# Optimization experiments

Hardware: AMD Instinct MI355X
Metric: run time of the kernel (lower is better)

The kernel has to match this reference:

```python
import jax, jax.numpy as jnp
import numpy as np

B, S, H, E, L = 8, 512, 768, 8, 2
SPAN, ATTR = 5, 31
EPS = 1e-5


def _layernorm(x, g, b):
    mu = jnp.mean(x, axis=-1, keepdims=True)
    var = jnp.mean(jnp.square(x - mu), axis=-1, keepdims=True)
    return g * (x - mu) * jax.lax.rsqrt(var + EPS) + b


def setup_inputs() -> dict:
    key = jax.random.key(0)
    ks = iter(jax.random.split(key, 32))

    def unif(k, shape, bound):
        return jax.random.uniform(k, shape, jnp.float32, -bound, bound)

    b3d = float(np.sqrt(6.0 / (H * E + H * E)))   # xavier for [H,H,E]
    bH = float(1.0 / np.sqrt(H))
    inp = {
        "share_hidden": jax.random.normal(next(ks), (B, S, H), jnp.float32),
        "span_hidden": jax.random.normal(next(ks), (B, S, H), jnp.float32),
        "attr_hidden": jax.random.normal(next(ks), (B, S, H), jnp.float32),
        # per-layer params stacked on leading axis L; expert axis order: (shared, task1, task2)
        "ln_g": jnp.ones((L, 3, H), jnp.float32),
        "ln_b": jnp.zeros((L, 3, H), jnp.float32),
        "W_exp": unif(next(ks), (L, 3, H, H, E), b3d),
        "b_exp": unif(next(ks), (L, 3, H, E), bH),
        "Wg_sh": unif(next(ks), (L, H, 3 * E), bH),
        "bg_sh": unif(next(ks), (L, 3 * E), bH),
        "Wg_t1": unif(next(ks), (L, H, 2 * E), bH),
        "bg_t1": unif(next(ks), (L, 2 * E), bH),
        "Wg_t2": unif(next(ks), (L, H, 2 * E), bH),
        "bg_t2": unif(next(ks), (L, 2 * E), bH),
        "W_span": unif(next(ks), (H, SPAN), bH),
        "b_span": unif(next(ks), (SPAN,), bH),
        "W_as": unif(next(ks), (H, ATTR), bH),
        "b_as": unif(next(ks), (ATTR,), bH),
        "W_ae": unif(next(ks), (H, ATTR), bH),
        "b_ae": unif(next(ks), (ATTR,), bH),
    }
    return inp


def reference(share_hidden, span_hidden, attr_hidden, ln_g, ln_b, W_exp, b_exp,
              Wg_sh, bg_sh, Wg_t1, bg_t1, Wg_t2, bg_t2,
              W_span, b_span, W_as, b_as, W_ae, b_ae):
    act = lambda x: jax.nn.gelu(x, approximate=False)  # torch F.gelu default is exact
    h_sh, h_t1, h_t2 = share_hidden, span_hidden, attr_hidden
    for l in range(L):
        x_sh = _layernorm(h_sh, ln_g[l, 0], ln_b[l, 0])
        x_t1 = _layernorm(h_t1, ln_g[l, 1], ln_b[l, 1])
        x_t2 = _layernorm(h_t2, ln_g[l, 2], ln_b[l, 2])
        # batched expert projections: [B,S,H] x [H,H,E] -> [B,S,H,E]
        e_sh = act(jnp.einsum('bsh,hxe->bsxe', x_sh, W_exp[l, 0]) + b_exp[l, 0])
        e_t1 = act(jnp.einsum('bsh,hxe->bsxe', x_t1, W_exp[l, 1]) + b_exp[l, 1])
        e_t2 = act(jnp.einsum('bsh,hxe->bsxe', x_t2, W_exp[l, 2]) + b_exp[l, 2])
        # gates
        g_sh = jax.nn.softmax(x_sh @ Wg_sh[l] + bg_sh[l], axis=-1)   # [B,S,3E]
        g_t1 = jax.nn.softmax(x_t1 @ Wg_t1[l] + bg_t1[l], axis=-1)   # [B,S,2E]
        g_t2 = jax.nn.softmax(x_t2 @ Wg_t2[l] + bg_t2[l], axis=-1)   # [B,S,2E]
        # weighted combine over concatenated expert axes (concat order matches torch code)
        o_sh = jnp.einsum('bse,bsxe->bsx', g_sh, jnp.concatenate([e_t1, e_sh, e_t2], axis=-1))
        o_t1 = jnp.einsum('bse,bsxe->bsx', g_t1, jnp.concatenate([e_t1, e_sh], axis=-1))
        o_t2 = jnp.einsum('bse,bsxe->bsx', g_t2, jnp.concatenate([e_t2, e_sh], axis=-1))
        # residual accumulation (progressive_layered_extraction)
        h_sh = h_sh + o_sh
        h_t1 = h_t1 + o_t1
        h_t2 = h_t2 + o_t2
    span_logits = h_t1 @ W_span + b_span
    attr_start_logits = h_t2 @ W_as + b_as
    attr_end_logits = h_t2 @ W_ae + b_ae
    return (span_logits, attr_start_logits, attr_end_logits)
```

## Files before the change

kernel.cpp:

```cpp
#include <hip/hip_runtime.h>
#include <hip/hip_bf16.h>
#include <math.h>

#define M_ 4096
#define N_ 6144
#define K_ 768
#define KP 832
#define H_ 768
#define L_ 2
#define NT 13

using bf16x8 = __attribute__((ext_vector_type(8))) short;
using f32x4  = __attribute__((ext_vector_type(4))) float;

__device__ __forceinline__ unsigned short f2bf(float f) {
  unsigned int u = __builtin_bit_cast(unsigned int, f);
  u += 0x7FFFu + ((u >> 16) & 1u);
  return (unsigned short)(u >> 16);
}

__device__ __forceinline__ float bf2f(unsigned short u) {
  return __builtin_bit_cast(float, (unsigned int)u << 16);
}

__device__ __forceinline__ float gelu_fast(float x) {
  float u2 = x * (1.5957691f + 0.07135481f * x * x);
  return x / (1.f + __expf(-u2));
}

__device__ __forceinline__ void gload_lds16(const void* g, void* l) {
  __builtin_amdgcn_global_load_lds(
      (__attribute__((address_space(1))) unsigned int*)(uintptr_t)g,
      (__attribute__((address_space(3))) unsigned int*)(unsigned int)(uintptr_t)l,
      16, 0, 0);
}

__global__ __launch_bounds__(256) void conv_w(const float* __restrict__ W,
                                              const float* __restrict__ bias,
                                              short* __restrict__ Wb) {
  __shared__ float tile[64][65];
  const int z = blockIdx.z;
  const int n0 = blockIdx.x * 64;
  const int k0 = blockIdx.y * 64;
  const size_t inb  = (size_t)z * K_ * N_;
  const size_t outb = (size_t)z * N_ * KP;
  const int tid = threadIdx.x;
  const int c = tid & 63;
  const int r = tid >> 6;
#pragma unroll
  for (int p = 0; p < 16; ++p) {
    const int kk = p * 4 + r;
    tile[c][kk] = W[inb + (size_t)(k0 + kk) * N_ + n0 + c];
  }
  __syncthreads();
#pragma unroll
  for (int p = 0; p < 16; ++p) {
    const int nn = p * 4 + r;
    Wb[outb + (size_t)(n0 + nn) * KP + k0 + c] = (short)f2bf(tile[nn][c]);
  }
  if (blockIdx.y == 0) {
    const int row = tid >> 2, c0 = (tid & 3) * 16;
    short* dst = Wb + outb + (size_t)(n0 + row) * KP + 768 + c0;
    ushort4 vz; vz.x = 0; vz.y = 0; vz.z = 0; vz.w = 0;
    ushort4 v0 = vz;
    if (c0 == 0) v0.x = f2bf(bias[(size_t)z * N_ + n0 + row]);
    *(ushort4*)dst = v0;
    *(ushort4*)(dst + 4) = vz;
    *(ushort4*)(dst + 8) = vz;
    *(ushort4*)(dst + 12) = vz;
  }
}

__global__ __launch_bounds__(256, 4) void ln_gates(
    const float* __restrict__ in0, const float* __restrict__ in1,
    const float* __restrict__ in2,
    float* __restrict__ h,
    const unsigned short* __restrict__ part,
    int mode,
    short* __restrict__ xs,
    const float* __restrict__ ln_g,
    const float* __restrict__ ln_b,
    const float* __restrict__ Wg_sh, const float* __restrict__ bg_sh,
    const float* __restrict__ Wg_t1, const float* __restrict__ bg_t1,
    const float* __restrict__ Wg_t2, const float* __restrict__ bg_t2,
    float* __restrict__ gates)
{
  const int gw   = blockIdx.x * 4 + (threadIdx.x >> 6);
  const int t    = gw >> 12;
  const int row  = gw & 4095;
  const int lane = threadIdx.x & 63;
  const float* srow = (t == 0 ? in0 : (t == 1 ? in1 : in2)) + (size_t)row * H_;
  float* hrow = h + ((size_t)t * M_ + row) * H_;

  const size_t MH = (size_t)M_ * H_;
  const unsigned short *pa = nullptr, *pb = nullptr, *pc = nullptr;
  if (mode) {
    if (t == 0)      { pa = part + (size_t)row * H_;          pb = part + 3 * MH + (size_t)row * H_; pc = part + 5 * MH + (size_t)row * H_; }
    else if (t == 1) { pa = part + 1 * MH + (size_t)row * H_; pb = part + 4 * MH + (size_t)row * H_; }
    else             { pa = part + 2 * MH + (size_t)row * H_; pb = part + 6 * MH + (size_t)row * H_; }
  }

  float x[12];
  float sum = 0.f, ss = 0.f;
#pragma unroll
  for (int q = 0; q < 3; ++q) {
    const int o = q * 256 + lane * 4;
    float4 v = *(const float4*)(srow + o);
    if (mode) {
      ushort4 a4 = *(const ushort4*)(pa + o);
      ushort4 b4 = *(const ushort4*)(pb + o);
      v.x += bf2f(a4.x) + bf2f(b4.x);
      v.y += bf2f(a4.y) + bf2f(b4.y);
      v.z += bf2f(a4.z) + bf2f(b4.z);
      v.w += bf2f(a4.w) + bf2f(b4.w);
      if (t == 0) {
        ushort4 c4 = *(const ushort4*)(pc + o);
        v.x += bf2f(c4.x); v.y += bf2f(c4.y); v.z += bf2f(c4.z); v.w += bf2f(c4.w);
      }
      *(float4*)(hrow + o) = v;
    }
    x[q * 4 + 0] = v.x; x[q * 4 + 1] = v.y; x[q * 4 + 2] = v.z; x[q * 4 + 3] = v.w;
    sum += v.x + v.y + v.z + v.w;
    ss  += v.x * v.x + v.y * v.y + v.z * v.z + v.w * v.w;
  }
#pragma unroll
  for (int m = 1; m < 64; m <<= 1) { sum += __shfl_xor(sum, m); ss += __shfl_xor(ss, m); }
  const float mean = sum * (1.f / 768.f);
  float var = ss * (1.f / 768.f) - mean * mean;
  var = var < 0.f ? 0.f : var;
  const float rstd = rsqrtf(var + 1e-5f);

  const float* ga = ln_g + (size_t)t * H_;
  const float* be = ln_b + (size_t)t * H_;
  short* xrow = xs + ((size_t)t * M_ + row) * KP;
#pragma unroll
  for (int q = 0; q < 3; ++q) {
    float4 g4 = *(const float4*)(ga + q * 256 + lane * 4);
    float4 b4 = *(const float4*)(be + q * 256 + lane * 4);
    float y0 = g4.x * (x[q * 4 + 0] - mean) * rstd + b4.x;
    float y1 = g4.y * (x[q * 4 + 1] - mean) * rstd + b4.y;
    float y2 = g4.z * (x[q * 4 + 2] - mean) * rstd + b4.z;
    float y3 = g4.w * (x[q * 4 + 3] - mean) * rstd + b4.w;
    x[q * 4 + 0] = y0; x[q * 4 + 1] = y1; x[q * 4 + 2] = y2; x[q * 4 + 3] = y3;
    ushort4 st; st.x = f2bf(y0); st.y = f2bf(y1); st.z = f2bf(y2); st.w = f2bf(y3);
    *(ushort4*)(xrow + q * 256 + lane * 4) = st;
  }
  if (lane < 16) {
    ushort4 z; z.x = (lane == 0) ? 0x3F80 : 0; z.y = 0; z.z = 0; z.w = 0;
    *(ushort4*)(xrow + 768 + lane * 4) = z;
  }

  const float* Wg; const float* bg;
  if (t == 0)      { Wg = Wg_sh; bg = bg_sh; }
  else if (t == 1) { Wg = Wg_t1; bg = bg_t1; }
  else             { Wg = Wg_t2; bg = bg_t2; }
  const int NG = (t == 0) ? 24 : 16;

  float p[24];
#pragma unroll
  for (int j = 0; j < 24; ++j) p[j] = 0.f;
#pragma unroll
  for (int q = 0; q < 3; ++q)
#pragma unroll
    for (int jj = 0; jj < 4; ++jj) {
      const int i = q * 256 + lane * 4 + jj;
      const float xv = x[q * 4 + jj];
      const float* wrow = Wg + (size_t)i * NG;
#pragma unroll
      for (int j = 0; j < 16; ++j) p[j] += xv * wrow[j];
      if (t == 0) {
#pragma unroll
        for (int j = 16; j < 24; ++j) p[j] += xv * wrow[j];
      }
    }
#pragma unroll
  for (int j = 0; j < 16; ++j)
#pragma unroll
    for (int m = 1; m < 64; m <<= 1) p[j] += __shfl_xor(p[j], m);
  if (t == 0) {
#pragma unroll
    for (int j = 16; j < 24; ++j)
#pragma unroll
      for (int m = 1; m < 64; m <<= 1) p[j] += __shfl_xor(p[j], m);
  }
  float mx = -1e30f;
#pragma unroll
  for (int j = 0; j < 16; ++j) { p[j] += bg[j]; mx = fmaxf(mx, p[j]); }
  if (t == 0) {
#pragma unroll
    for (int j = 16; j < 24; ++j) { p[j] += bg[j]; mx = fmaxf(mx, p[j]); }
  }
  float s = 0.f;
#pragma unroll
  for (int j = 0; j < 16; ++j) { p[j] = __expf(p[j] - mx); s += p[j]; }
  if (t == 0) {
#pragma unroll
    for (int j = 16; j < 24; ++j) { p[j] = __expf(p[j] - mx); s += p[j]; }
  }
  const float inv = 1.f / s;

  float* grow;
  if (t == 0)      grow = gates + (size_t)row * 24;
  else if (t == 1) grow = gates + (size_t)M_ * 24 + (size_t)row * 16;
  else             grow = gates + (size_t)M_ * 24 + (size_t)M_ * 16 + (size_t)row * 16;
  if (lane == 0) {
#pragma unroll
    for (int j = 0; j < 16; ++j) grow[j] = p[j] * inv;
    if (t == 0) {
#pragma unroll
      for (int j = 16; j < 24; ++j) grow[j] = p[j] * inv;
    }
  }
}

__global__ __launch_bounds__(256, 3) void expert_gemm(
    const short* __restrict__ xs,
    const short* __restrict__ Wb,
    const float* __restrict__ g_sh,
    const float* __restrict__ g_t1,
    const float* __restrict__ g_t2,
    unsigned short* __restrict__ part)
{
  __shared__ short lds[16384];

  const int bid = blockIdx.x;
  const int xcd = bid & 7;
  const int idx = bid >> 3;
  const int t   = idx / 192;
  const int r2  = idx - t * 192;
  const int mt  = r2 / 6;
  const int m0  = mt * 128;
  const int n0  = (xcd * 6 + (r2 - mt * 6)) * 128;

  const short* A  = xs + (size_t)t * M_ * KP;
  const short* Bt = Wb + (size_t)t * N_ * KP;

  const int tid = threadIdx.x;
  const int w = tid >> 6, l = tid & 63;
  const int wr = w >> 1, wc = w & 1;

  const int lr = l & 15, cg = l >> 4;
  const int fx = lr >> 1;
  const int slot0 = ((cg ^ fx) << 3);
  const int slot1 = (((4 + cg) ^ fx) << 3);
  const int aoff = wr * 4096 + lr * 64;
  const int boff = 8192 + wc * 4096 + lr * 64;

  f32x4 acc[4][4];
#pragma unroll
  for (int i = 0; i < 4; ++i)
#pragma unroll
    for (int j = 0; j < 4; ++j) acc[i][j] = (f32x4){0.f, 0.f, 0.f, 0.f};

  for (int kt = 0; kt < NT; ++kt) {
    __syncthreads();
#pragma unroll
    for (int q = 0; q < 4; ++q) {
      const int row = w * 32 + q * 8 + (l >> 3);
      const int fq = (q * 4 + (l >> 4)) & 7;
      const int csw = ((l & 7) ^ fq) << 3;
      gload_lds16(A  + (size_t)(m0 + row) * KP + kt * 64 + csw, &lds[(w * 32 + q * 8) * 64]);
      gload_lds16(Bt + (size_t)(n0 + row) * KP + kt * 64 + csw, &lds[8192 + (w * 32 + q * 8) * 64]);
    }
    __syncthreads();

    bf16x8 a[4][2], b[4][2];
#pragma unroll
    for (int fm = 0; fm < 4; ++fm) {
      a[fm][0] = *(const bf16x8*)&lds[aoff + fm * 1024 + slot0];
      a[fm][1] = *(const bf16x8*)&lds[aoff + fm * 1024 + slot1];
    }
#pragma unroll
    for (int fn = 0; fn < 4; ++fn) {
      b[fn][0] = *(const bf16x8*)&lds[boff + fn * 1024 + slot0];
      b[fn][1] = *(const bf16x8*)&lds[boff + fn * 1024 + slot1];
    }
    __builtin_amdgcn_s_setprio(1);
#pragma unroll
    for (int ks = 0; ks < 2; ++ks)
#pragma unroll
      for (int fm = 0; fm < 4; ++fm)
#pragma unroll
        for (int fn = 0; fn < 4; ++fn)
          acc[fm][fn] = __builtin_amdgcn_mfma_f32_16x16x32_bf16(a[fm][ks], b[fn][ks], acc[fm][fn], 0, 0, 0);
    __builtin_amdgcn_s_setprio(0);
  }
  __syncthreads();

  const size_t MH = (size_t)M_ * H_;
  const float *gpA, *gpB, *gpC = nullptr;
  unsigned short *ppA, *ppB, *ppC = nullptr;
  int ldA, ldB, ldC = 16, offA, offB, offC = 0, ntg;
  if (t == 0) {
    gpA = g_sh; ldA = 24; offA = 8; ppA = part;
    gpB = g_t1; ldB = 16; offB = 8; ppB = part + 1 * MH;
    gpC = g_t2; ldC = 16; offC = 8; ppC = part + 2 * MH; ntg = 3;
  } else if (t == 1) {
    gpA = g_sh; ldA = 24; offA = 0; ppA = part + 3 * MH;
    gpB = g_t1; ldB = 16; offB = 0; ppB = part + 4 * MH; ntg = 2;
  } else {
    gpA = g_sh; ldA = 24; offA = 16; ppA = part + 5 * MH;
    gpB = g_t2; ldB = 16; offB = 0;  ppB = part + 6 * MH; ntg = 2;
  }
  float* wtile = (float*)lds + w * 1040;
  const int xbase = (n0 + wc * 64) >> 3;
  const int xloc = l & 7;

#pragma unroll
  for (int fm = 0; fm < 4; ++fm) {
    asm volatile("s_waitcnt lgkmcnt(0)" ::: "memory");
#pragma unroll
    for (int fn = 0; fn < 4; ++fn)
#pragma unroll
      for (int r = 0; r < 4; ++r)
        wtile[(cg * 4 + r) * 65 + fn * 16 + lr] = gelu_fast(acc[fm][fn][r]);
    asm volatile("s_waitcnt lgkmcnt(0)" ::: "memory");

    float v[2][8];
    int gm[2];
#pragma unroll
    for (int p = 0; p < 2; ++p) {
      const int mloc = p * 8 + (l >> 3);
      float4 v0 = *(const float4*)&wtile[mloc * 65 + xloc * 8];
      float4 v1 = *(const float4*)&wtile[mloc * 65 + xloc * 8 + 4];
      v[p][0] = v0.x; v[p][1] = v0.y; v[p][2] = v0.z; v[p][3] = v0.w;
      v[p][4] = v1.x; v[p][5] = v1.y; v[p][6] = v1.z; v[p][7] = v1.w;
      gm[p] = m0 + wr * 64 + fm * 16 + mloc;
    }

#define DO_STREAM(gp, ldg, offg, pp)                                          \
    {                                                                         \
      _Pragma("unroll")                                                       \
      for (int p = 0; p < 2; ++p) {                                           \
        const float* gr = (gp) + (size_t)gm[p] * (ldg) + (offg);              \
        float4 ga = *(const float4*)gr;                                       \
        float4 gb = *(const float4*)(gr + 4);                                 \
        float o = ga.x * v[p][0] + ga.y * v[p][1] + ga.z * v[p][2]            \
                + ga.w * v[p][3] + gb.x * v[p][4] + gb.y * v[p][5]            \
                + gb.z * v[p][6] + gb.w * v[p][7];                            \
        (pp)[(size_t)gm[p] * H_ + xbase + xloc] = f2bf(o);                    \
      }                                                                       \
    }
    DO_STREAM(gpA, ldA, offA, ppA);
    DO_STREAM(gpB, ldB, offB, ppB);
    if (ntg == 3) DO_STREAM(gpC, ldC, offC, ppC);
#undef DO_STREAM
  }
}

__global__ __launch_bounds__(128) void heads(
    const float* __restrict__ h,
    const unsigned short* __restrict__ part,
    const float* __restrict__ Wspan, const float* __restrict__ bspan,
    const float* __restrict__ Was,   const float* __restrict__ bas,
    const float* __restrict__ Wae,   const float* __restrict__ bae,
    float* __restrict__ out)
{
  const int row = blockIdx.x;
  __shared__ float s1[768], s2[768];
  const size_t MH = (size_t)M_ * H_;
  const float* h1 = h + ((size_t)M_ + row) * H_;
  const float* h2 = h + ((size_t)2 * M_ + row) * H_;
  const unsigned short* p1a = part + 1 * MH + (size_t)row * H_;
  const unsigned short* p1b = part + 4 * MH + (size_t)row * H_;
  const unsigned short* p2a = part + 2 * MH + (size_t)row * H_;
  const unsigned short* p2b = part + 6 * MH + (size_t)row * H_;
  for (int i = threadIdx.x; i < 768; i += 128) {
    s1[i] = h1[i] + bf2f(p1a[i]) + bf2f(p1b[i]);
    s2[i] = h2[i] + bf2f(p2a[i]) + bf2f(p2b[i]);
  }
  __syncthreads();
  const int j = threadIdx.x;
  const float* W; const float* src; float bias; float* op; int ldw;
  if (j < 5)       { W = Wspan + j;      src = s1; bias = bspan[j];  op = out + (size_t)row * 5 + j;                ldw = 5;  }
  else if (j < 36) { W = Was + (j - 5);  src = s2; bias = bas[j-5];  op = out + 20480 + (size_t)row * 31 + (j-5);   ldw = 31; }
  else if (j < 67) { W = Wae + (j - 36); src = s2; bias = bae[j-36]; op = out + 147456 + (size_t)row * 31 + (j-36); ldw = 31; }
  else return;
  float acc = bias;
  for (int i = 0; i < 768; ++i) acc += src[i] * W[(size_t)i * ldw];
  *op = acc;
}

extern "C" void kernel_launch(void* const* d_in, const int* in_sizes, int n_in,
                              void* d_out, int out_size, void* d_ws, size_t ws_size,
                              hipStream_t stream) {
  (void)in_sizes; (void)n_in; (void)out_size; (void)ws_size;
  const float* share  = (const float*)d_in[0];
  const float* span   = (const float*)d_in[1];
  const float* attr   = (const float*)d_in[2];
  const float* ln_g   = (const float*)d_in[3];
  const float* ln_b   = (const float*)d_in[4];
  const float* W_exp  = (const float*)d_in[5];
  const float* b_exp  = (const float*)d_in[6];
  const float* Wg_sh  = (const float*)d_in[7];
  const float* bg_sh  = (const float*)d_in[8];
  const float* Wg_t1  = (const float*)d_in[9];
  const float* bg_t1  = (const float*)d_in[10];
  const float* Wg_t2  = (const float*)d_in[11];
  const float* bg_t2  = (const float*)d_in[12];
  const float* W_span = (const float*)d_in[13];
  const float* b_span = (const float*)d_in[14];
  const float* W_as   = (const float*)d_in[15];
  const float* b_as   = (const float*)d_in[16];
  const float* W_ae   = (const float*)d_in[17];
  const float* b_ae   = (const float*)d_in[18];

  char* ws = (char*)d_ws;
  short* Wb = (short*)ws;
  size_t o = (size_t)3 * N_ * KP * 2;
  short* xs = (short*)(ws + o); o += (size_t)3 * M_ * KP * 2;
  float* h  = (float*)(ws + o); o += (size_t)3 * M_ * H_ * 4;
  float* gates = (float*)(ws + o); o += (size_t)M_ * (24 + 16 + 16) * 4;
  unsigned short* part = (unsigned short*)(ws + o);

  for (int l = 0; l < L_; ++l) {
    conv_w<<<dim3(96, 12, 3), 256, 0, stream>>>(
        W_exp + (size_t)l * 3 * K_ * N_, b_exp + (size_t)l * 3 * N_, Wb);
    ln_gates<<<3072, 256, 0, stream>>>(
        share, span, attr, h, part, l, xs,
        ln_g + (size_t)l * 3 * H_, ln_b + (size_t)l * 3 * H_,
        Wg_sh + (size_t)l * H_ * 24, bg_sh + (size_t)l * 24,
        Wg_t1 + (size_t)l * H_ * 16, bg_t1 + (size_t)l * 16,
        Wg_t2 + (size_t)l * H_ * 16, bg_t2 + (size_t)l * 16,
        gates);
    expert_gemm<<<4608, 256, 0, stream>>>(
        xs, Wb,
        gates, gates + (size_t)M_ * 24, gates + (size_t)M_ * 24 + (size_t)M_ * 16,
        part);
  }

  heads<<<4096, 128, 0, stream>>>(h, part, W_span, b_span, W_as, b_as, W_ae, b_ae,
                                  (float*)d_out);
}
```

Before: 591.8 us.

## Widen expert GEMM tile to 128x256 with triple-buffered async LDS pipeline

Doubles the expert GEMM block tile along N (128x256) and halves the K step to 32. The K loop becomes a three-stage ring buffer: global-to-LDS loads for step kt+2 are issued while step kt is computed, and vmcnt waits with a single barrier replace the two syncthreads per iteration. The goal is to hide global load latency and raise MFMA work per byte loaded. In exchange, LDS grows to about 72 KB and registers to 32 accumulators per wave, so occupancy drops to 2 blocks per CU and the grid is halved. The epilogue is remapped to the wider tile.

```diff
diff --git a/kernel.cpp b/kernel.cpp
--- a/kernel.cpp
+++ b/kernel.cpp
@@ -8,7 +8,7 @@
 #define KP 832
 #define H_ 768
 #define L_ 2
-#define NT 13
+#define NT 26
 
 using bf16x8 = __attribute__((ext_vector_type(8))) short;
 using f32x4  = __attribute__((ext_vector_type(4))) float;
@@ -213,7 +213,7 @@
   }
 }
 
-__global__ __launch_bounds__(256, 3) void expert_gemm(
+__global__ __launch_bounds__(256, 2) void expert_gemm(
     const short* __restrict__ xs,
     const short* __restrict__ Wb,
     const float* __restrict__ g_sh,
@@ -221,69 +221,83 @@
     const float* __restrict__ g_t2,
     unsigned short* __restrict__ part)
 {
-  __shared__ short lds[16384];
+  __shared__ short lds[36864];
 
   const int bid = blockIdx.x;
   const int xcd = bid & 7;
   const int idx = bid >> 3;
-  const int t   = idx / 192;
-  const int r2  = idx - t * 192;
-  const int mt  = r2 / 6;
+  const int t   = idx / 96;
+  const int r2  = idx - t * 96;
+  const int mt  = r2 / 3;
   const int m0  = mt * 128;
-  const int n0  = (xcd * 6 + (r2 - mt * 6)) * 128;
+  const int n0  = (xcd * 3 + (r2 - mt * 3)) * 256;
 
   const short* A  = xs + (size_t)t * M_ * KP;
   const short* Bt = Wb + (size_t)t * N_ * KP;
 
   const int tid = threadIdx.x;
   const int w = tid >> 6, l = tid & 63;
-  const int wr = w >> 1, wc = w & 1;
+  const int wr = w & 1, wc = w >> 1;
+
+  const int csw = (((l & 3) ^ ((l >> 3) & 3)) << 3);
+  const int lrow = l >> 2;
+  const short* As0 = A  + (size_t)(m0 +       w * 16 + lrow) * KP + csw;
+  const short* As1 = A  + (size_t)(m0 +  64 + w * 16 + lrow) * KP + csw;
+  const short* Bs0 = Bt + (size_t)(n0 +       w * 16 + lrow) * KP + csw;
+  const short* Bs1 = Bt + (size_t)(n0 +  64 + w * 16 + lrow) * KP + csw;
+  const short* Bs2 = Bt + (size_t)(n0 + 128 + w * 16 + lrow) * KP + csw;
+  const short* Bs3 = Bt + (size_t)(n0 + 192 + w * 16 + lrow) * KP + csw;
+  const int dstw = w * 512;
+
+  auto stage = [&](int kt) {
+    const int bb = (kt % 3) * 12288;
+    const int ko = kt * 32;
+    gload_lds16(As0 + ko, &lds[bb + dstw]);
+    gload_lds16(As1 + ko, &lds[bb + 2048 + dstw]);
+    gload_lds16(Bs0 + ko, &lds[bb + 4096 + dstw]);
+    gload_lds16(Bs1 + ko, &lds[bb + 6144 + dstw]);
+    gload_lds16(Bs2 + ko, &lds[bb + 8192 + dstw]);
+    gload_lds16(Bs3 + ko, &lds[bb + 10240 + dstw]);
+  };
 
   const int lr = l & 15, cg = l >> 4;
-  const int fx = lr >> 1;
-  const int slot0 = ((cg ^ fx) << 3);
-  const int slot1 = (((4 + cg) ^ fx) << 3);
-  const int aoff = wr * 4096 + lr * 64;
-  const int boff = 8192 + wc * 4096 + lr * 64;
-
-  f32x4 acc[4][4];
+  const int slot = ((cg ^ ((lr >> 1) & 3)) << 3);
+  const int aoff = (wr * 64 + lr) * 32 + slot;
+  const int boff = 4096 + (wc * 128 + lr) * 32 + slot;
+
+  f32x4 acc[4][8];
 #pragma unroll
   for (int i = 0; i < 4; ++i)
 #pragma unroll
-    for (int j = 0; j < 4; ++j) acc[i][j] = (f32x4){0.f, 0.f, 0.f, 0.f};
+    for (int j = 0; j < 8; ++j) acc[i][j] = (f32x4){0.f, 0.f, 0.f, 0.f};
+
+  stage(0); stage(1);
+  asm volatile("s_waitcnt vmcnt(6)" ::: "memory");
+  __builtin_amdgcn_s_barrier();
 
   for (int kt = 0; kt < NT; ++kt) {
-    __syncthreads();
-#pragma unroll
-    for (int q = 0; q < 4; ++q) {
-      const int row = w * 32 + q * 8 + (l >> 3);
-      const int fq = (q * 4 + (l >> 4)) & 7;
-      const int csw = ((l & 7) ^ fq) << 3;
-      gload_lds16(A  + (size_t)(m0 + row) * KP + kt * 64 + csw, &lds[(w * 32 + q * 8) * 64]);
-      gload_lds16(Bt + (size_t)(n0 + row) * KP + kt * 64 + csw, &lds[8192 + (w * 32 + q * 8) * 64]);
+    if (kt + 2 < NT) stage(kt + 2);
+    __builtin_amdgcn_sched_barrier(0);
+
+    const int bb = (kt % 3) * 12288;
+    bf16x8 a[4], b[8];
+#pragma unroll
+    for (int fm = 0; fm < 4; ++fm) a[fm] = *(const bf16x8*)&lds[bb + aoff + fm * 512];
+#pragma unroll
+    for (int fn = 0; fn < 8; ++fn) b[fn] = *(const bf16x8*)&lds[bb + boff + fn * 512];
+    __builtin_amdgcn_s_setprio(1);
+#pragma unroll
+    for (int fm = 0; fm < 4; ++fm)
+#pragma unroll
+      for (int fn = 0; fn < 8; ++fn)
+        acc[fm][fn] = __builtin_amdgcn_mfma_f32_16x16x32_bf16(a[fm], b[fn], acc[fm][fn], 0, 0, 0);
+    __builtin_amdgcn_s_setprio(0);
+
+    if (kt < NT - 1) {
+      if (kt + 2 < NT) asm volatile("s_waitcnt vmcnt(6)" ::: "memory");
+      else             asm volatile("s_waitcnt vmcnt(0)" ::: "memory");
+      __builtin_amdgcn_s_barrier();
     }
-    __syncthreads();
-
-    bf16x8 a[4][2], b[4][2];
-#pragma unroll
-    for (int fm = 0; fm < 4; ++fm) {
-      a[fm][0] = *(const bf16x8*)&lds[aoff + fm * 1024 + slot0];
-      a[fm][1] = *(const bf16x8*)&lds[aoff + fm * 1024 + slot1];
-    }
-#pragma unroll
-    for (int fn = 0; fn < 4; ++fn) {
-      b[fn][0] = *(const bf16x8*)&lds[boff + fn * 1024 + slot0];
-      b[fn][1] = *(const bf16x8*)&lds[boff + fn * 1024 + slot1];
-    }
-    __builtin_amdgcn_s_setprio(1);
-#pragma unroll
-    for (int ks = 0; ks < 2; ++ks)
-#pragma unroll
-      for (int fm = 0; fm < 4; ++fm)
-#pragma unroll
-        for (int fn = 0; fn < 4; ++fn)
-          acc[fm][fn] = __builtin_amdgcn_mfma_f32_16x16x32_bf16(a[fm][ks], b[fn][ks], acc[fm][fn], 0, 0, 0);
-    __builtin_amdgcn_s_setprio(0);
   }
   __syncthreads();
 
@@ -302,49 +316,41 @@
     gpA = g_sh; ldA = 24; offA = 16; ppA = part + 5 * MH;
     gpB = g_t2; ldB = 16; offB = 0;  ppB = part + 6 * MH; ntg = 2;
   }
-  float* wtile = (float*)lds + w * 1040;
-  const int xbase = (n0 + wc * 64) >> 3;
-  const int xloc = l & 7;
+  float* wtile = (float*)lds + w * 2112;
+  const int xloc = l >> 2;
+  const int mfr  = l & 3;
+  const int xcol = ((n0 + wc * 128) >> 3) + xloc;
 
 #pragma unroll
   for (int fm = 0; fm < 4; ++fm) {
     asm volatile("s_waitcnt lgkmcnt(0)" ::: "memory");
 #pragma unroll
-    for (int fn = 0; fn < 4; ++fn)
+    for (int fn = 0; fn < 8; ++fn)
 #pragma unroll
       for (int r = 0; r < 4; ++r)
-        wtile[(cg * 4 + r) * 65 + fn * 16 + lr] = gelu_fast(acc[fm][fn][r]);
+        wtile[(cg * 4 + r) * 132 + fn * 16 + lr] = gelu_fast(acc[fm][fn][r]);
     asm volatile("s_waitcnt lgkmcnt(0)" ::: "memory");
 
-    float v[2][8];
-    int gm[2];
-#pragma unroll
-    for (int p = 0; p < 2; ++p) {
-      const int mloc = p * 8 + (l >> 3);
-      float4 v0 = *(const float4*)&wtile[mloc * 65 + xloc * 8];
-      float4 v1 = *(const float4*)&wtile[mloc * 65 + xloc * 8 + 4];
-      v[p][0] = v0.x; v[p][1] = v0.y; v[p][2] = v0.z; v[p][3] = v0.w;
-      v[p][4] = v1.x; v[p][5] = v1.y; v[p][6] = v1.z; v[p][7] = v1.w;
-      gm[p] = m0 + wr * 64 + fm * 16 + mloc;
-    }
-
+#pragma unroll
+    for (int p = 0; p < 4; ++p) {
+      const int mloc = p * 4 + mfr;
+      const int gm = m0 + wr * 64 + fm * 16 + mloc;
+      float4 v0 = *(const float4*)&wtile[mloc * 132 + xloc * 8];
+      float4 v1 = *(const float4*)&wtile[mloc * 132 + xloc * 8 + 4];
 #define DO_STREAM(gp, ldg, offg, pp)                                          \
-    {                                                                         \
-      _Pragma("unroll")                                                       \
-      for (int p = 0; p < 2; ++p) {                                           \
-        const float* gr = (gp) + (size_t)gm[p] * (ldg) + (offg);              \
+      {                                                                       \
+        const float* gr = (gp) + (size_t)gm * (ldg) + (offg);                 \
         float4 ga = *(const float4*)gr;                                       \
         float4 gb = *(const float4*)(gr + 4);                                 \
-        float o = ga.x * v[p][0] + ga.y * v[p][1] + ga.z * v[p][2]            \
-                + ga.w * v[p][3] + gb.x * v[p][4] + gb.y * v[p][5]            \
-                + gb.z * v[p][6] + gb.w * v[p][7];                            \
-        (pp)[(size_t)gm[p] * H_ + xbase + xloc] = f2bf(o);                    \
-      }                                                                       \
+        float o = ga.x * v0.x + ga.y * v0.y + ga.z * v0.z + ga.w * v0.w       \
+                + gb.x * v1.x + gb.y * v1.y + gb.z * v1.z + gb.w * v1.w;      \
+        (pp)[(size_t)gm * H_ + xcol] = f2bf(o);                               \
+      }
+      DO_STREAM(gpA, ldA, offA, ppA);
+      DO_STREAM(gpB, ldB, offB, ppB);
+      if (ntg == 3) DO_STREAM(gpC, ldC, offC, ppC);
+#undef DO_STREAM
     }
-    DO_STREAM(gpA, ldA, offA, ppA);
-    DO_STREAM(gpB, ldB, offB, ppB);
-    if (ntg == 3) DO_STREAM(gpC, ldC, offC, ppC);
-#undef DO_STREAM
   }
 }
 
@@ -423,7 +429,7 @@
         Wg_t1 + (size_t)l * H_ * 16, bg_t1 + (size_t)l * 16,
         Wg_t2 + (size_t)l * H_ * 16, bg_t2 + (size_t)l * 16,
         gates);
-    expert_gemm<<<4608, 256, 0, stream>>>(
+    expert_gemm<<<2304, 256, 0, stream>>>(
         xs, Wb,
         gates, gates + (size_t)M_ * 24, gates + (size_t)M_ * 24 + (size_t)M_ * 16,
         part);
```

Measured after the change: 620.5 us. +4.8%, slower.

## Triple-buffer expert GEMM LDS tiles with async prefetch two stages ahead

Applied to the files above, without the earlier changes.

Replaces the load-then-sync loop of the expert GEMM with a 3-stage ring buffer in LDS. Each stage now covers a K-slice of 32 instead of 64, and global-to-LDS loads are issued two iterations ahead. Explicit vmcnt waits plus a single barrier per iteration replace the two __syncthreads. This is meant to hide global memory latency behind the MFMAs. In exchange it doubles the iteration count, uses 48KB of LDS instead of 32KB (which may limit occupancy at 3 blocks per CU), and changes the swizzle pattern.

```diff
diff --git a/kernel.cpp b/kernel.cpp
--- a/kernel.cpp
+++ b/kernel.cpp
@@ -8,7 +8,7 @@
 #define KP 832
 #define H_ 768
 #define L_ 2
-#define NT 13
+#define NT 26
 
 using bf16x8 = __attribute__((ext_vector_type(8))) short;
 using f32x4  = __attribute__((ext_vector_type(4))) float;
@@ -221,7 +221,7 @@
     const float* __restrict__ g_t2,
     unsigned short* __restrict__ part)
 {
-  __shared__ short lds[16384];
+  __shared__ short lds[24576];
 
   const int bid = blockIdx.x;
   const int xcd = bid & 7;
@@ -239,12 +239,27 @@
   const int w = tid >> 6, l = tid & 63;
   const int wr = w >> 1, wc = w & 1;
 
+  const int csw = (((l & 3) ^ ((l >> 3) & 3)) << 3);
+  const int lrow = l >> 2;
+  const short* As0 = A  + (size_t)(m0 +      w * 16 + lrow) * KP + csw;
+  const short* As1 = A  + (size_t)(m0 + 64 + w * 16 + lrow) * KP + csw;
+  const short* Bs0 = Bt + (size_t)(n0 +      w * 16 + lrow) * KP + csw;
+  const short* Bs1 = Bt + (size_t)(n0 + 64 + w * 16 + lrow) * KP + csw;
+  const int dstw = w * 512;
+
+  auto stage = [&](int kt) {
+    const int bb = (kt % 3) * 8192;
+    const int ko = kt * 32;
+    gload_lds16(As0 + ko, &lds[bb + dstw]);
+    gload_lds16(As1 + ko, &lds[bb + 2048 + dstw]);
+    gload_lds16(Bs0 + ko, &lds[bb + 4096 + dstw]);
+    gload_lds16(Bs1 + ko, &lds[bb + 6144 + dstw]);
+  };
+
   const int lr = l & 15, cg = l >> 4;
-  const int fx = lr >> 1;
-  const int slot0 = ((cg ^ fx) << 3);
-  const int slot1 = (((4 + cg) ^ fx) << 3);
-  const int aoff = wr * 4096 + lr * 64;
-  const int boff = 8192 + wc * 4096 + lr * 64;
+  const int slot = ((cg ^ ((lr >> 1) & 3)) << 3);
+  const int aoff = (wr * 64 + lr) * 32 + slot;
+  const int boff = 4096 + (wc * 64 + lr) * 32 + slot;
 
   f32x4 acc[4][4];
 #pragma unroll
@@ -252,38 +267,33 @@
 #pragma unroll
     for (int j = 0; j < 4; ++j) acc[i][j] = (f32x4){0.f, 0.f, 0.f, 0.f};
 
+  stage(0); stage(1);
+  asm volatile("s_waitcnt vmcnt(4)" ::: "memory");
+  __builtin_amdgcn_s_barrier();
+
   for (int kt = 0; kt < NT; ++kt) {
-    __syncthreads();
-#pragma unroll
-    for (int q = 0; q < 4; ++q) {
-      const int row = w * 32 + q * 8 + (l >> 3);
-      const int fq = (q * 4 + (l >> 4)) & 7;
-      const int csw = ((l & 7) ^ fq) << 3;
-      gload_lds16(A  + (size_t)(m0 + row) * KP + kt * 64 + csw, &lds[(w * 32 + q * 8) * 64]);
-      gload_lds16(Bt + (size_t)(n0 + row) * KP + kt * 64 + csw, &lds[8192 + (w * 32 + q * 8) * 64]);
-    }
-    __syncthreads();
-
-    bf16x8 a[4][2], b[4][2];
-#pragma unroll
-    for (int fm = 0; fm < 4; ++fm) {
-      a[fm][0] = *(const bf16x8*)&lds[aoff + fm * 1024 + slot0];
-      a[fm][1] = *(const bf16x8*)&lds[aoff + fm * 1024 + slot1];
-    }
-#pragma unroll
-    for (int fn = 0; fn < 4; ++fn) {
-      b[fn][0] = *(const bf16x8*)&lds[boff + fn * 1024 + slot0];
-      b[fn][1] = *(const bf16x8*)&lds[boff + fn * 1024 + slot1];
-    }
+    if (kt + 2 < NT) stage(kt + 2);
+    __builtin_amdgcn_sched_barrier(0);
+
+    const int bb = (kt % 3) * 8192;
+    bf16x8 a[4], b[4];
+#pragma unroll
+    for (int fm = 0; fm < 4; ++fm) a[fm] = *(const bf16x8*)&lds[bb + aoff + fm * 512];
+#pragma unroll
+    for (int fn = 0; fn < 4; ++fn) b[fn] = *(const bf16x8*)&lds[bb + boff + fn * 512];
     __builtin_amdgcn_s_setprio(1);
 #pragma unroll
-    for (int ks = 0; ks < 2; ++ks)
-#pragma unroll
-      for (int fm = 0; fm < 4; ++fm)
-#pragma unroll
-        for (int fn = 0; fn < 4; ++fn)
-          acc[fm][fn] = __builtin_amdgcn_mfma_f32_16x16x32_bf16(a[fm][ks], b[fn][ks], acc[fm][fn], 0, 0, 0);
+    for (int fm = 0; fm < 4; ++fm)
+#pragma unroll
+      for (int fn = 0; fn < 4; ++fn)
+        acc[fm][fn] = __builtin_amdgcn_mfma_f32_16x16x32_bf16(a[fm], b[fn], acc[fm][fn], 0, 0, 0);
     __builtin_amdgcn_s_setprio(0);
+
+    if (kt < NT - 1) {
+      if (kt + 2 < NT) asm volatile("s_waitcnt vmcnt(4) lgkmcnt(0)" ::: "memory");
+      else             asm volatile("s_waitcnt vmcnt(0) lgkmcnt(0)" ::: "memory");
+      __builtin_amdgcn_s_barrier();
+    }
   }
   __syncthreads();
 
```

Measured after the change: 623.3 us. +5.3%, slower.

## Stage gate weights in LDS as transposed bf16 and process two rows per wave

Applied to the files above, without the earlier changes.

The ln_gates kernel now loads each task's gate weight matrix once per block into shared memory, transposed and converted to bf16, so that each lane reads contiguous weights for its 12 input elements. Previously every lane read strided fp32 gate rows from global memory for each row. Each block now covers 8 rows (two per wave) and the grid is halved, which spreads the staging cost over more rows. In exchange it adds a block-level staging pass, 36KB of LDS per block, and bf16 rounding of the gate weights, which may slightly change the softmax outputs.

```diff
diff --git a/kernel.cpp b/kernel.cpp
--- a/kernel.cpp
+++ b/kernel.cpp
@@ -68,6 +68,38 @@
     *(ushort4*)(dst + 4) = vz;
     *(ushort4*)(dst + 8) = vz;
     *(ushort4*)(dst + 12) = vz;
+  }
+}
+
+template<int NG>
+__device__ __forceinline__ void gate_sm(const float x[12],
+    const unsigned short* Wlds, const float* __restrict__ bg,
+    float* __restrict__ grow, int lane) {
+  float p[NG];
+#pragma unroll
+  for (int j = 0; j < NG; ++j) {
+    const unsigned short* wr = Wlds + j * 768 + lane * 4;
+    ushort4 wa = *(const ushort4*)wr;
+    ushort4 wb = *(const ushort4*)(wr + 256);
+    ushort4 wc = *(const ushort4*)(wr + 512);
+    p[j] = bf2f(wa.x) * x[0] + bf2f(wa.y) * x[1] + bf2f(wa.z) * x[2]  + bf2f(wa.w) * x[3]
+         + bf2f(wb.x) * x[4] + bf2f(wb.y) * x[5] + bf2f(wb.z) * x[6]  + bf2f(wb.w) * x[7]
+         + bf2f(wc.x) * x[8] + bf2f(wc.y) * x[9] + bf2f(wc.z) * x[10] + bf2f(wc.w) * x[11];
+  }
+#pragma unroll
+  for (int j = 0; j < NG; ++j)
+#pragma unroll
+    for (int m = 1; m < 64; m <<= 1) p[j] += __shfl_xor(p[j], m);
+  float mx = -1e30f;
+#pragma unroll
+  for (int j = 0; j < NG; ++j) { p[j] += bg[j]; mx = fmaxf(mx, p[j]); }
+  float s = 0.f;
+#pragma unroll
+  for (int j = 0; j < NG; ++j) { p[j] = __expf(p[j] - mx); s += p[j]; }
+  const float inv = 1.f / s;
+  if (lane == 0) {
+#pragma unroll
+    for (int j = 0; j < NG; ++j) grow[j] = p[j] * inv;
   }
 }
 
@@ -85,130 +117,108 @@
     const float* __restrict__ Wg_t2, const float* __restrict__ bg_t2,
     float* __restrict__ gates)
 {
-  const int gw   = blockIdx.x * 4 + (threadIdx.x >> 6);
-  const int t    = gw >> 12;
-  const int row  = gw & 4095;
-  const int lane = threadIdx.x & 63;
-  const float* srow = (t == 0 ? in0 : (t == 1 ? in1 : in2)) + (size_t)row * H_;
-  float* hrow = h + ((size_t)t * M_ + row) * H_;
+  __shared__ unsigned short Wlds[24 * 768];
+
+  const int b = blockIdx.x;
+  const int t = b >> 9;
+  const int rbase = (b & 511) * 8;
+  const int w = threadIdx.x >> 6, lane = threadIdx.x & 63;
+
+  if (t == 0) {
+    for (int i4 = threadIdx.x; i4 < 768 * 24 / 4; i4 += 256) {
+      float4 v = ((const float4*)Wg_sh)[i4];
+      const int e0 = i4 * 4;
+#pragma unroll
+      for (int k2 = 0; k2 < 4; ++k2) {
+        const int e = e0 + k2, i = e / 24, j = e - i * 24;
+        Wlds[j * 768 + i] = f2bf(((const float*)&v)[k2]);
+      }
+    }
+  } else {
+    const float* Wg = (t == 1) ? Wg_t1 : Wg_t2;
+    for (int i4 = threadIdx.x; i4 < 768 * 16 / 4; i4 += 256) {
+      float4 v = ((const float4*)Wg)[i4];
+      const int e0 = i4 * 4;
+#pragma unroll
+      for (int k2 = 0; k2 < 4; ++k2) {
+        const int e = e0 + k2;
+        Wlds[(e & 15) * 768 + (e >> 4)] = f2bf(((const float*)&v)[k2]);
+      }
+    }
+  }
+  __syncthreads();
 
   const size_t MH = (size_t)M_ * H_;
-  const unsigned short *pa = nullptr, *pb = nullptr, *pc = nullptr;
-  if (mode) {
-    if (t == 0)      { pa = part + (size_t)row * H_;          pb = part + 3 * MH + (size_t)row * H_; pc = part + 5 * MH + (size_t)row * H_; }
-    else if (t == 1) { pa = part + 1 * MH + (size_t)row * H_; pb = part + 4 * MH + (size_t)row * H_; }
-    else             { pa = part + 2 * MH + (size_t)row * H_; pb = part + 6 * MH + (size_t)row * H_; }
-  }
-
-  float x[12];
-  float sum = 0.f, ss = 0.f;
-#pragma unroll
-  for (int q = 0; q < 3; ++q) {
-    const int o = q * 256 + lane * 4;
-    float4 v = *(const float4*)(srow + o);
+  const float* inp = (t == 0) ? in0 : (t == 1) ? in1 : in2;
+
+  for (int r = 0; r < 2; ++r) {
+    const int row = rbase + w * 2 + r;
+    const float* srow = inp + (size_t)row * H_;
+    float* hrow = h + ((size_t)t * M_ + row) * H_;
+
+    const unsigned short *pa = nullptr, *pb = nullptr, *pc = nullptr;
     if (mode) {
-      ushort4 a4 = *(const ushort4*)(pa + o);
-      ushort4 b4 = *(const ushort4*)(pb + o);
-      v.x += bf2f(a4.x) + bf2f(b4.x);
-      v.y += bf2f(a4.y) + bf2f(b4.y);
-      v.z += bf2f(a4.z) + bf2f(b4.z);
-      v.w += bf2f(a4.w) + bf2f(b4.w);
-      if (t == 0) {
-        ushort4 c4 = *(const ushort4*)(pc + o);
-        v.x += bf2f(c4.x); v.y += bf2f(c4.y); v.z += bf2f(c4.z); v.w += bf2f(c4.w);
+      if (t == 0)      { pa = part + (size_t)row * H_;          pb = part + 3 * MH + (size_t)row * H_; pc = part + 5 * MH + (size_t)row * H_; }
+      else if (t == 1) { pa = part + 1 * MH + (size_t)row * H_; pb = part + 4 * MH + (size_t)row * H_; }
+      else             { pa = part + 2 * MH + (size_t)row * H_; pb = part + 6 * MH + (size_t)row * H_; }
+    }
+
+    float x[12];
+    float sum = 0.f, ss = 0.f;
+#pragma unroll
+    for (int q = 0; q < 3; ++q) {
+      const int o = q * 256 + lane * 4;
+      float4 v = *(const float4*)(srow + o);
+      if (mode) {
+        ushort4 a4 = *(const ushort4*)(pa + o);
+        ushort4 b4 = *(const ushort4*)(pb + o);
+        v.x += bf2f(a4.x) + bf2f(b4.x);
+        v.y += bf2f(a4.y) + bf2f(b4.y);
+        v.z += bf2f(a4.z) + bf2f(b4.z);
+        v.w += bf2f(a4.w) + bf2f(b4.w);
+        if (t == 0) {
+          ushort4 c4 = *(const ushort4*)(pc + o);
+          v.x += bf2f(c4.x); v.y += bf2f(c4.y); v.z += bf2f(c4.z); v.w += bf2f(c4.w);
+        }
+        *(float4*)(hrow + o) = v;
       }
-      *(float4*)(hrow + o) = v;
-    }
-    x[q * 4 + 0] = v.x; x[q * 4 + 1] = v.y; x[q * 4 + 2] = v.z; x[q * 4 + 3] = v.w;
-    sum += v.x + v.y + v.z + v.w;
-    ss  += v.x * v.x + v.y * v.y + v.z * v.z + v.w * v.w;
-  }
-#pragma unroll
-  for (int m = 1; m < 64; m <<= 1) { sum += __shfl_xor(sum, m); ss += __shfl_xor(ss, m); }
-  const float mean = sum * (1.f / 768.f);
-  float var = ss * (1.f / 768.f) - mean * mean;
-  var = var < 0.f ? 0.f : var;
-  const float rstd = rsqrtf(var + 1e-5f);
-
-  const float* ga = ln_g + (size_t)t * H_;
-  const float* be = ln_b + (size_t)t * H_;
-  short* xrow = xs + ((size_t)t * M_ + row) * KP;
-#pragma unroll
-  for (int q = 0; q < 3; ++q) {
-    float4 g4 = *(const float4*)(ga + q * 256 + lane * 4);
-    float4 b4 = *(const float4*)(be + q * 256 + lane * 4);
-    float y0 = g4.x * (x[q * 4 + 0] - mean) * rstd + b4.x;
-    float y1 = g4.y * (x[q * 4 + 1] - mean) * rstd + b4.y;
-    float y2 = g4.z * (x[q * 4 + 2] - mean) * rstd + b4.z;
-    float y3 = g4.w * (x[q * 4 + 3] - mean) * rstd + b4.w;
-    x[q * 4 + 0] = y0; x[q * 4 + 1] = y1; x[q * 4 + 2] = y2; x[q * 4 + 3] = y3;
-    ushort4 st; st.x = f2bf(y0); st.y = f2bf(y1); st.z = f2bf(y2); st.w = f2bf(y3);
-    *(ushort4*)(xrow + q * 256 + lane * 4) = st;
-  }
-  if (lane < 16) {
-    ushort4 z; z.x = (lane == 0) ? 0x3F80 : 0; z.y = 0; z.z = 0; z.w = 0;
-    *(ushort4*)(xrow + 768 + lane * 4) = z;
-  }
-
-  const float* Wg; const float* bg;
-  if (t == 0)      { Wg = Wg_sh; bg = bg_sh; }
-  else if (t == 1) { Wg = Wg_t1; bg = bg_t1; }
-  else             { Wg = Wg_t2; bg = bg_t2; }
-  const int NG = (t == 0) ? 24 : 16;
-
-  float p[24];
-#pragma unroll
-  for (int j = 0; j < 24; ++j) p[j] = 0.f;
-#pragma unroll
-  for (int q = 0; q < 3; ++q)
-#pragma unroll
-    for (int jj = 0; jj < 4; ++jj) {
-      const int i = q * 256 + lane * 4 + jj;
-      const float xv = x[q * 4 + jj];
-      const float* wrow = Wg + (size_t)i * NG;
-#pragma unroll
-      for (int j = 0; j < 16; ++j) p[j] += xv * wrow[j];
-      if (t == 0) {
-#pragma unroll
-        for (int j = 16; j < 24; ++j) p[j] += xv * wrow[j];
-      }
-    }
-#pragma unroll
-  for (int j = 0; j < 16; ++j)
-#pragma unroll
-    for (int m = 1; m < 64; m <<= 1) p[j] += __shfl_xor(p[j], m);
-  if (t == 0) {
-#pragma unroll
-    for (int j = 16; j < 24; ++j)
-#pragma unroll
-      for (int m = 1; m < 64; m <<= 1) p[j] += __shfl_xor(p[j], m);
-  }
-  float mx = -1e30f;
-#pragma unroll
-  for (int j = 0; j < 16; ++j) { p[j] += bg[j]; mx = fmaxf(mx, p[j]); }
-  if (t == 0) {
-#pragma unroll
-    for (int j = 16; j < 24; ++j) { p[j] += bg[j]; mx = fmaxf(mx, p[j]); }
-  }
-  float s = 0.f;
-#pragma unroll
-  for (int j = 0; j < 16; ++j) { p[j] = __expf(p[j] - mx); s += p[j]; }
-  if (t == 0) {
-#pragma unroll
-    for (int j = 16; j < 24; ++j) { p[j] = __expf(p[j] - mx); s += p[j]; }
-  }
-  const float inv = 1.f / s;
-
-  float* grow;
-  if (t == 0)      grow = gates + (size_t)row * 24;
-  else if (t == 1) grow = gates + (size_t)M_ * 24 + (size_t)row * 16;
-  else             grow = gates + (size_t)M_ * 24 + (size_t)M_ * 16 + (size_t)row * 16;
-  if (lane == 0) {
-#pragma unroll
-    for (int j = 0; j < 16; ++j) grow[j] = p[j] * inv;
+      x[q * 4 + 0] = v.x; x[q * 4 + 1] = v.y; x[q * 4 + 2] = v.z; x[q * 4 + 3] = v.w;
+      sum += v.x + v.y + v.z + v.w;
+      ss  += v.x * v.x + v.y * v.y + v.z * v.z + v.w * v.w;
+    }
+#pragma unroll
+    for (int m = 1; m < 64; m <<= 1) { sum += __shfl_xor(sum, m); ss += __shfl_xor(ss, m); }
+    const float mean = sum * (1.f / 768.f);
+    float var = ss * (1.f / 768.f) - mean * mean;
+    var = var < 0.f ? 0.f : var;
+    const float rstd = rsqrtf(var + 1e-5f);
+
+    const float* ga = ln_g + (size_t)t * H_;
+    const float* be = ln_b + (size_t)t * H_;
+    short* xrow = xs + ((size_t)t * M_ + row) * KP;
+#pragma unroll
+    for (int q = 0; q < 3; ++q) {
+      float4 g4 = *(const float4*)(ga + q * 256 + lane * 4);
+      float4 b4 = *(const float4*)(be + q * 256 + lane * 4);
+      float y0 = g4.x * (x[q * 4 + 0] - mean) * rstd + b4.x;
+      float y1 = g4.y * (x[q * 4 + 1] - mean) * rstd + b4.y;
+      float y2 = g4.z * (x[q * 4 + 2] - mean) * rstd + b4.z;
+      float y3 = g4.w * (x[q * 4 + 3] - mean) * rstd + b4.w;
+      x[q * 4 + 0] = y0; x[q * 4 + 1] = y1; x[q * 4 + 2] = y2; x[q * 4 + 3] = y3;
+      ushort4 st; st.x = f2bf(y0); st.y = f2bf(y1); st.z = f2bf(y2); st.w = f2bf(y3);
+      *(ushort4*)(xrow + q * 256 + lane * 4) = st;
+    }
+    if (lane < 16) {
+      ushort4 z; z.x = (lane == 0) ? 0x3F80 : 0; z.y = 0; z.z = 0; z.w = 0;
+      *(ushort4*)(xrow + 768 + lane * 4) = z;
+    }
+
     if (t == 0) {
-#pragma unroll
-      for (int j = 16; j < 24; ++j) grow[j] = p[j] * inv;
+      gate_sm<24>(x, Wlds, bg_sh, gates + (size_t)row * 24, lane);
+    } else if (t == 1) {
+      gate_sm<16>(x, Wlds, bg_t1, gates + (size_t)M_ * 24 + (size_t)row * 16, lane);
+    } else {
+      gate_sm<16>(x, Wlds, bg_t2, gates + (size_t)M_ * 24 + (size_t)M_ * 16 + (size_t)row * 16, lane);
     }
   }
 }
@@ -416,7 +426,7 @@
   for (int l = 0; l < L_; ++l) {
     conv_w<<<dim3(96, 12, 3), 256, 0, stream>>>(
         W_exp + (size_t)l * 3 * K_ * N_, b_exp + (size_t)l * 3 * N_, Wb);
-    ln_gates<<<3072, 256, 0, stream>>>(
+    ln_gates<<<1536, 256, 0, stream>>>(
         share, span, attr, h, part, l, xs,
         ln_g + (size_t)l * 3 * H_, ln_b + (size_t)l * 3 * H_,
         Wg_sh + (size_t)l * H_ * 24, bg_sh + (size_t)l * 24,
```

After: 505.6 us. 14.6% less time.
